# Optimization experiments

Measured on AMD Instinct MI355X. Metric: run time of the kernel, lower is better.

Reference implementation:

```python
import jax, jax.numpy as jnp
import numpy as np

D_MODEL = 1024
HEADS = 16
DILATION = 4
LN_EPS = 1e-5


def setup_inputs() -> dict:
    key = jax.random.key(0)
    ks = jax.random.split(key, 11)
    B, S, D = 2, 4096, D_MODEL
    x = jax.random.normal(ks[0], (B, S, D), dtype=jnp.float32)
    def lin(k):
        kw, kb = jax.random.split(k)
        W = jax.random.normal(kw, (D, D), dtype=jnp.float32) * 0.02  # torch Linear layout [out, in]
        b = jax.random.normal(kb, (D,), dtype=jnp.float32) * 0.02
        return W, b
    Wq, bq = lin(ks[1])
    Wk, bk = lin(ks[2])
    Wv, bv = lin(ks[3])
    Wf, bf = lin(ks[4])
    gamma = jnp.ones((D,), dtype=jnp.float32)
    beta = jnp.zeros((D,), dtype=jnp.float32)
    return {"x": x, "Wq": Wq, "bq": bq, "Wk": Wk, "bk": bk,
            "Wv": Wv, "bv": bv, "Wf": Wf, "bf": bf,
            "gamma": gamma, "beta": beta}


def _layer_norm(x, gamma, beta):
    mu = jnp.mean(x, axis=-1, keepdims=True)
    var = jnp.mean(jnp.square(x - mu), axis=-1, keepdims=True)
    return (x - mu) * jax.lax.rsqrt(var + LN_EPS) * gamma + beta


def reference(x, Wq, bq, Wk, bk, Wv, bv, Wf, bf, gamma, beta):
    B, S, D = x.shape
    dil, H = DILATION, HEADS
    dh = D // H
    pad = (-S) % dil  # padding_size
    xp = jnp.pad(x, ((0, 0), (0, pad), (0, 0)))
    Sp = S + pad
    L = Sp // dil
    # strided (atrous) regrouping: [B, Sp, D] -> [B*dil, L, D]
    xr = xp.reshape(B, L, dil, D).transpose(0, 2, 1, 3).reshape(B * dil, L, D)
    q = xr @ Wq.T + bq
    k = xr @ Wk.T + bk
    v = xr @ Wv.T + bv
    # split heads: [B*dil, H, L, dh]
    q = q.reshape(B * dil, L, H, dh).transpose(0, 2, 1, 3)
    k = k.reshape(B * dil, L, H, dh).transpose(0, 2, 1, 3)
    v = v.reshape(B * dil, L, H, dh).transpose(0, 2, 1, 3)
    scores = jnp.einsum('bhqd,bhkd->bhqk', q, k) / jnp.sqrt(jnp.float32(dh))
    probs = jax.nn.softmax(scores, axis=-1)
    ctx = jnp.einsum('bhqk,bhkd->bhqd', probs, v)
    # merge heads and undo atrous regrouping
    ctx = ctx.transpose(0, 2, 1, 3).reshape(B * dil, L, D)
    ctx = ctx.reshape(B, dil, L, D).transpose(0, 2, 1, 3).reshape(B, Sp, D)
    ctx = ctx[:, :S]
    atted = ctx @ Wf.T + bf  # dropout p=0.0
    final = _layer_norm(atted + x, gamma, beta)
    return (final, atted)
```

## Files before the change

### kernel.cpp

```cpp
#include <hip/hip_runtime.h>
#include <hip/hip_bf16.h>
#include <cstdint>
#include <cstddef>

constexpr int B_  = 2;
constexpr int S_  = 4096;
constexpr int D_  = 1024;
constexpr int H_  = 16;
constexpr int DH_ = 64;
constexpr int DIL = 4;
constexpr int L_  = S_ / DIL;
constexpr int M_  = B_ * S_;

typedef __attribute__((ext_vector_type(8))) short short8;
typedef __attribute__((ext_vector_type(4))) float f32x4;

__device__ __forceinline__ unsigned short f2b(float f) {
    union { float f; unsigned u; } v;
    v.f = f;
    unsigned r = v.u + 0x7fff + ((v.u >> 16) & 1);
    return (unsigned short)(r >> 16);
}

__device__ __forceinline__ unsigned pkbf(float a, float b) {
    float2 t; t.x = a; t.y = b;
    __hip_bfloat162 h = __float22bfloat162_rn(t);
    union { __hip_bfloat162 h; unsigned u; } c; c.h = h;
    return c.u;
}

__device__ __forceinline__ int xcd_swz(int orig, int nwg) {
    int q = nwg >> 3, r = nwg & 7;
    int xcd = orig & 7, idx = orig >> 3;
    return (xcd < r ? xcd * (q + 1) : r * (q + 1) + (xcd - r) * q) + idx;
}

#define GLOAD16(gptr, lptr)                                                    \
    __builtin_amdgcn_global_load_lds(                                          \
        (const __attribute__((address_space(1))) void*)(gptr),                 \
        (__attribute__((address_space(3))) void*)(lptr), 16, 0, 0)

__global__ __launch_bounds__(256)
void conv_f2b(const float* __restrict__ in, unsigned short* __restrict__ out, int n4) {
    int i = blockIdx.x * 256 + threadIdx.x;
    if (i < n4) {
        float4 v = reinterpret_cast<const float4*>(in)[i];
        ushort4 o;
        o.x = f2b(v.x); o.y = f2b(v.y); o.z = f2b(v.z); o.w = f2b(v.w);
        reinterpret_cast<ushort4*>(out)[i] = o;
    }
}

__global__ __launch_bounds__(256)
void conv_w4(const float* __restrict__ w0, const float* __restrict__ w1,
             const float* __restrict__ w2, const float* __restrict__ w3,
             unsigned short* __restrict__ out) {
    int bid = blockIdx.x;
    int which = bid >> 10;
    const float* src = (which == 0) ? w0 : (which == 1) ? w1 : (which == 2) ? w2 : w3;
    int i = (bid & 1023) * 256 + threadIdx.x;
    float4 v = reinterpret_cast<const float4*>(src)[i];
    ushort4 o;
    o.x = f2b(v.x); o.y = f2b(v.y); o.z = f2b(v.z); o.w = f2b(v.w);
    reinterpret_cast<ushort4*>(out + (size_t)which * D_ * D_)[i] = o;
}

template <int OUT_BF16>
__global__ __launch_bounds__(256)
void gemm_mfma(const unsigned short* __restrict__ A,
               const unsigned short* __restrict__ W,
               const float* __restrict__ bias,
               void* __restrict__ Cout, int M, int N, int K) {
    __shared__ unsigned short As[128 * 64];
    __shared__ unsigned short Bs[128 * 64];

    const int tid  = threadIdx.x;
    const int lane = tid & 63, wave = tid >> 6;
    const int l15 = lane & 15, l4 = lane >> 4;
    const int wr = wave >> 1, wc = wave & 1;
    const int gx = N >> 7;
    const int wg = xcd_swz(blockIdx.x, gridDim.x);
    const int bm = (wg / gx) * 128, bn = (wg % gx) * 128;

    f32x4 acc[4][4] = {};

    for (int k0 = 0; k0 < K; k0 += 64) {
        #pragma unroll
        for (int i = 0; i < 4; ++i) {
            int ch = i * 256 + wave * 64 + lane;
            int r = ch >> 3, c8 = ch & 7;
            const unsigned short* ga = A + (size_t)(bm + r) * K + k0 + c8 * 8;
            GLOAD16(ga, (char*)As + (size_t)(i * 256 + wave * 64) * 16);
            const unsigned short* gb = W + (size_t)(bn + r) * K + k0 + c8 * 8;
            GLOAD16(gb, (char*)Bs + (size_t)(i * 256 + wave * 64) * 16);
        }
        __syncthreads();

        #pragma unroll
        for (int ks = 0; ks < 2; ++ks) {
            short8 af[4], bf[4];
            #pragma unroll
            for (int mi = 0; mi < 4; ++mi)
                af[mi] = *reinterpret_cast<const short8*>(
                    &As[(wr * 64 + mi * 16 + l15) * 64 + ks * 32 + l4 * 8]);
            #pragma unroll
            for (int ni = 0; ni < 4; ++ni)
                bf[ni] = *reinterpret_cast<const short8*>(
                    &Bs[(wc * 64 + ni * 16 + l15) * 64 + ks * 32 + l4 * 8]);
            #pragma unroll
            for (int mi = 0; mi < 4; ++mi)
                #pragma unroll
                for (int ni = 0; ni < 4; ++ni)
                    acc[mi][ni] = __builtin_amdgcn_mfma_f32_16x16x32_bf16(
                        af[mi], bf[ni], acc[mi][ni], 0, 0, 0);
        }
        __syncthreads();
    }

    #pragma unroll
    for (int ni = 0; ni < 4; ++ni) {
        int col = bn + wc * 64 + ni * 16 + l15;
        float bv = bias[col];
        #pragma unroll
        for (int mi = 0; mi < 4; ++mi) {
            #pragma unroll
            for (int r = 0; r < 4; ++r) {
                int row = bm + wr * 64 + mi * 16 + l4 * 4 + r;
                float v = acc[mi][ni][r] + bv;
                if (OUT_BF16)
                    ((unsigned short*)Cout)[(size_t)row * N + col] = f2b(v);
                else
                    ((float*)Cout)[(size_t)row * N + col] = v;
            }
        }
    }
}

__global__ __launch_bounds__(256)
void gemm_qkv(const unsigned short* __restrict__ A,
              const unsigned short* __restrict__ W,
              const float* __restrict__ bq, const float* __restrict__ bk,
              const float* __restrict__ bv,
              unsigned short* __restrict__ Qb, unsigned short* __restrict__ Kb,
              unsigned short* __restrict__ Vb, int M, int K) {
    __shared__ unsigned short As[128 * 64];
    __shared__ unsigned short Bs[128 * 64];

    const int tid  = threadIdx.x;
    const int lane = tid & 63, wave = tid >> 6;
    const int l15 = lane & 15, l4 = lane >> 4;
    const int wr = wave >> 1, wc = wave & 1;
    const int gx = 24;
    const int wg = xcd_swz(blockIdx.x, gridDim.x);
    const int bm = (wg / gx) * 128, bn = (wg % gx) * 128;

    f32x4 acc[4][4] = {};

    for (int k0 = 0; k0 < K; k0 += 64) {
        #pragma unroll
        for (int i = 0; i < 4; ++i) {
            int ch = i * 256 + wave * 64 + lane;
            int r = ch >> 3, c8 = ch & 7;
            const unsigned short* ga = A + (size_t)(bm + r) * K + k0 + c8 * 8;
            GLOAD16(ga, (char*)As + (size_t)(i * 256 + wave * 64) * 16);
            const unsigned short* gb = W + (size_t)(bn + r) * K + k0 + c8 * 8;
            GLOAD16(gb, (char*)Bs + (size_t)(i * 256 + wave * 64) * 16);
        }
        __syncthreads();

        #pragma unroll
        for (int ks = 0; ks < 2; ++ks) {
            short8 af[4], bf[4];
            #pragma unroll
            for (int mi = 0; mi < 4; ++mi)
                af[mi] = *reinterpret_cast<const short8*>(
                    &As[(wr * 64 + mi * 16 + l15) * 64 + ks * 32 + l4 * 8]);
            #pragma unroll
            for (int ni = 0; ni < 4; ++ni)
                bf[ni] = *reinterpret_cast<const short8*>(
                    &Bs[(wc * 64 + ni * 16 + l15) * 64 + ks * 32 + l4 * 8]);
            #pragma unroll
            for (int mi = 0; mi < 4; ++mi)
                #pragma unroll
                for (int ni = 0; ni < 4; ++ni)
                    acc[mi][ni] = __builtin_amdgcn_mfma_f32_16x16x32_bf16(
                        af[mi], bf[ni], acc[mi][ni], 0, 0, 0);
        }
        __syncthreads();
    }

    const int seg = bn >> 10;
    const float* bp = (seg == 0) ? bq : (seg == 1) ? bk : bv;
    unsigned short* ob = (seg == 0) ? Qb : (seg == 1) ? Kb : Vb;
    const float qs = (seg == 0) ? 0.125f : 1.0f;
    const int cb = bn & 1023;

    #pragma unroll
    for (int ni = 0; ni < 4; ++ni) {
        int col = cb + wc * 64 + ni * 16 + l15;
        float bvv = bp[col];
        #pragma unroll
        for (int mi = 0; mi < 4; ++mi) {
            #pragma unroll
            for (int r = 0; r < 4; ++r) {
                int row = bm + wr * 64 + mi * 16 + l4 * 4 + r;
                ob[(size_t)row * 1024 + col] = f2b((acc[mi][ni][r] + bvv) * qs);
            }
        }
    }
}

__global__ __launch_bounds__(256)
void tvt(const unsigned short* __restrict__ Vb, unsigned short* __restrict__ Vtg) {
    __shared__ unsigned short Ts[64 * 64];
    const int tid = threadIdx.x;
    const int blk = blockIdx.x;
    const int lt = blk & 15;
    const int h  = (blk >> 4) & 15;
    const int bd = blk >> 8;
    const int b = bd >> 2, dd = bd & 3;
    const size_t rowbase = (size_t)b * S_;

    #pragma unroll
    for (int i = 0; i < 2; ++i) {
        int ch = i * 256 + tid;
        int lloc = ch >> 3, c8 = ch & 7;
        short8 v = *reinterpret_cast<const short8*>(
            Vb + (rowbase + (size_t)(lt * 64 + lloc) * DIL + dd) * D_ + h * 64 + c8 * 8);
        #pragma unroll
        for (int j = 0; j < 8; ++j) {
            int dh = c8 * 8 + j;
            Ts[dh * 64 + (((lloc >> 3) ^ (dh & 7)) * 8) + (lloc & 7)] = (unsigned short)v[j];
        }
    }
    __syncthreads();

    const size_t obase = ((size_t)(bd * 16 + h) * 64) * L_;
    #pragma unroll
    for (int i = 0; i < 2; ++i) {
        int ch = i * 256 + tid;
        int dh = ch >> 3, c = ch & 7;
        uint4 val = *reinterpret_cast<const uint4*>(&Ts[dh * 64 + ((c ^ (dh & 7)) * 8)]);
        *reinterpret_cast<uint4*>(Vtg + obase + (size_t)dh * L_ + lt * 64 + c * 8) = val;
    }
}

__global__ __launch_bounds__(256)
void attn_mfma(const unsigned short* __restrict__ Q,
               const unsigned short* __restrict__ K,
               const unsigned short* __restrict__ Vtg,
               unsigned short* __restrict__ O) {
    __shared__ unsigned short Ks[2][64 * 64];
    __shared__ unsigned short Vs[2][64 * 64];
    __shared__ unsigned short Ps[4][1024];

    const int tid = threadIdx.x;
    const int lane = tid & 63, wave = tid >> 6;
    const int l15 = lane & 15, l4 = lane >> 4;
    const int blk = xcd_swz(blockIdx.x, gridDim.x);
    const int qt = blk & 15;
    const int h  = (blk >> 4) & 15;
    const int bd = blk >> 8;
    const int b = bd >> 2, dd = bd & 3;
    const size_t rowbase = (size_t)b * S_;
    const int colbase = h * DH_;

    short8 qf[2];
    {
        int q = qt * 64 + wave * 16 + l15;
        const unsigned short* qp =
            Q + (rowbase + (size_t)q * DIL + dd) * D_ + colbase;
        qf[0] = *reinterpret_cast<const short8*>(qp + l4 * 8);
        qf[1] = *reinterpret_cast<const short8*>(qp + 32 + l4 * 8);
    }

    const unsigned short* vbase = Vtg + ((size_t)(bd * 16 + h) * 64) * L_;

    auto stageK = [&](int kt, int buf) {
        #pragma unroll
        for (int i = 0; i < 2; ++i) {
            int key = i * 32 + wave * 8 + (lane >> 3);
            int srcc = (lane & 7) ^ (lane >> 3);
            const unsigned short* g =
                K + (rowbase + (size_t)(kt * 64 + key) * DIL + dd) * D_ + colbase + srcc * 8;
            GLOAD16(g, (char*)&Ks[buf][0] + (size_t)(i * 256 + wave * 64) * 16);
        }
    };
    auto stageV = [&](int kt, int buf) {
        #pragma unroll
        for (int i = 0; i < 2; ++i) {
            int dh = i * 32 + wave * 8 + (lane >> 3);
            int srcc = (lane & 7) ^ (lane >> 3);
            const unsigned short* g = vbase + (size_t)dh * L_ + kt * 64 + srcc * 8;
            GLOAD16(g, (char*)&Vs[buf][0] + (size_t)(i * 256 + wave * 64) * 16);
        }
    };

    f32x4 oT[4] = {};
    float m_run = -1e30f, l_run = 0.f;

    stageK(0, 0);
    stageV(0, 0);
    __syncthreads();

    constexpr int NT = L_ / 64;
    for (int kt = 0; kt < NT; ++kt) {
        int cur = kt & 1, nxt = cur ^ 1;
        if (kt < NT - 1) {
            stageK(kt + 1, nxt);
            stageV(kt + 1, nxt);
        }

        f32x4 sT[4];
        #pragma unroll
        for (int n = 0; n < 4; ++n) {
            int row = n * 16 + l15;
            short8 kf0 = *reinterpret_cast<const short8*>(
                &Ks[cur][row * 64 + ((0 * 4 + l4) ^ (l15 & 7)) * 8]);
            short8 kf1 = *reinterpret_cast<const short8*>(
                &Ks[cur][row * 64 + ((1 * 4 + l4) ^ (l15 & 7)) * 8]);
            f32x4 z = {0.f, 0.f, 0.f, 0.f};
            z = __builtin_amdgcn_mfma_f32_16x16x32_bf16(kf0, qf[0], z, 0, 0, 0);
            z = __builtin_amdgcn_mfma_f32_16x16x32_bf16(kf1, qf[1], z, 0, 0, 0);
            sT[n] = z;
        }

        float mx = -1e30f;
        #pragma unroll
        for (int n = 0; n < 4; ++n)
            #pragma unroll
            for (int r = 0; r < 4; ++r) mx = fmaxf(mx, sT[n][r]);
        mx = fmaxf(mx, __shfl_xor(mx, 16));
        mx = fmaxf(mx, __shfl_xor(mx, 32));
        float m_new = fmaxf(m_run, mx);
        float scale = __expf(m_run - m_new);
        float p[4][4], rsum = 0.f;
        #pragma unroll
        for (int n = 0; n < 4; ++n)
            #pragma unroll
            for (int r = 0; r < 4; ++r) {
                p[n][r] = __expf(sT[n][r] - m_new);
                rsum += p[n][r];
            }
        rsum += __shfl_xor(rsum, 16);
        rsum += __shfl_xor(rsum, 32);
        l_run = l_run * scale + rsum;
        m_run = m_new;
        #pragma unroll
        for (int nd = 0; nd < 4; ++nd) oT[nd] *= scale;

        #pragma unroll
        for (int n = 0; n < 4; ++n) {
            uint2 w;
            w.x = pkbf(p[n][0], p[n][1]);
            w.y = pkbf(p[n][2], p[n][3]);
            int c = n * 2 + (l4 >> 1);
            int pc = c ^ (l15 & 7);
            *reinterpret_cast<uint2*>(&Ps[wave][l15 * 64 + pc * 8 + (l4 & 1) * 4]) = w;
        }
        short8 pb0 = *reinterpret_cast<const short8*>(
            &Ps[wave][l15 * 64 + ((0 * 4 + l4) ^ (l15 & 7)) * 8]);
        short8 pb1 = *reinterpret_cast<const short8*>(
            &Ps[wave][l15 * 64 + ((1 * 4 + l4) ^ (l15 & 7)) * 8]);

        #pragma unroll
        for (int ks = 0; ks < 2; ++ks) {
            short8 pb = ks ? pb1 : pb0;
            #pragma unroll
            for (int nd = 0; nd < 4; ++nd) {
                short8 vf = *reinterpret_cast<const short8*>(
                    &Vs[cur][(nd * 16 + l15) * 64 + ((ks * 4 + l4) ^ (l15 & 7)) * 8]);
                oT[nd] = __builtin_amdgcn_mfma_f32_16x16x32_bf16(vf, pb, oT[nd], 0, 0, 0);
            }
        }

        __syncthreads();
    }

    unsigned short* Es = &Ps[0][0];
    float inv = 1.f / l_run;
    #pragma unroll
    for (int nd = 0; nd < 4; ++nd) {
        uint2 w;
        w.x = pkbf(oT[nd][0] * inv, oT[nd][1] * inv);
        w.y = pkbf(oT[nd][2] * inv, oT[nd][3] * inv);
        int chunk = nd * 2 + (l4 >> 1);
        int pc = chunk ^ (l15 & 7);
        *reinterpret_cast<uint2*>(&Es[wave * 1024 + l15 * 64 + pc * 8 + (l4 & 1) * 4]) = w;
    }
    __syncthreads();
    {
        int row = lane >> 2;
        int q = qt * 64 + wave * 16 + row;
        unsigned short* op = O + (rowbase + (size_t)q * DIL + dd) * D_ + colbase;
        #pragma unroll
        for (int i = 0; i < 2; ++i) {
            int c = (lane & 3) * 2 + i;
            int pc = c ^ (row & 7);
            uint4 val = *reinterpret_cast<const uint4*>(&Es[wave * 1024 + row * 64 + pc * 8]);
            *reinterpret_cast<uint4*>(op + c * 8) = val;
        }
    }
}

__global__ __launch_bounds__(256)
void add_ln(const float* __restrict__ atted, const float* __restrict__ x,
            const float* __restrict__ gamma, const float* __restrict__ beta,
            float* __restrict__ out) {
    __shared__ float red[8];
    const int tid = threadIdx.x;
    const size_t base = (size_t)blockIdx.x * D_;

    float4 a  = *reinterpret_cast<const float4*>(atted + base + tid * 4);
    float4 xv = *reinterpret_cast<const float4*>(x + base + tid * 4);
    float v0 = a.x + xv.x, v1 = a.y + xv.y, v2 = a.z + xv.z, v3 = a.w + xv.w;

    float s = v0 + v1 + v2 + v3;
    #pragma unroll
    for (int o = 1; o < 64; o <<= 1) s += __shfl_xor(s, o);
    if ((tid & 63) == 0) red[tid >> 6] = s;
    __syncthreads();
    float mean = (red[0] + red[1] + red[2] + red[3]) * (1.0f / D_);

    float d0 = v0 - mean, d1 = v1 - mean, d2 = v2 - mean, d3 = v3 - mean;
    float sq = d0 * d0 + d1 * d1 + d2 * d2 + d3 * d3;
    #pragma unroll
    for (int o = 1; o < 64; o <<= 1) sq += __shfl_xor(sq, o);
    if ((tid & 63) == 0) red[4 + (tid >> 6)] = sq;
    __syncthreads();
    float var = (red[4] + red[5] + red[6] + red[7]) * (1.0f / D_);
    float inv = rsqrtf(var + 1e-5f);

    float4 g  = *reinterpret_cast<const float4*>(gamma + tid * 4);
    float4 bb = *reinterpret_cast<const float4*>(beta + tid * 4);
    float4 o4;
    o4.x = d0 * inv * g.x + bb.x;
    o4.y = d1 * inv * g.y + bb.y;
    o4.z = d2 * inv * g.z + bb.z;
    o4.w = d3 * inv * g.w + bb.w;
    *reinterpret_cast<float4*>(out + base + tid * 4) = o4;
}

extern "C" void kernel_launch(void* const* d_in, const int* in_sizes, int n_in,
                              void* d_out, int out_size, void* d_ws, size_t ws_size,
                              hipStream_t stream) {
    const float* x     = (const float*)d_in[0];
    const float* Wq    = (const float*)d_in[1];
    const float* bq    = (const float*)d_in[2];
    const float* Wk    = (const float*)d_in[3];
    const float* bk    = (const float*)d_in[4];
    const float* Wv    = (const float*)d_in[5];
    const float* bv    = (const float*)d_in[6];
    const float* Wf    = (const float*)d_in[7];
    const float* bf    = (const float*)d_in[8];
    const float* gamma = (const float*)d_in[9];
    const float* beta  = (const float*)d_in[10];

    float* final_out = (float*)d_out;
    float* atted     = final_out + (size_t)M_ * D_;

    unsigned short* xb  = (unsigned short*)d_ws;
    unsigned short* Wqb = xb  + (size_t)M_ * D_;
    unsigned short* Wkb = Wqb + (size_t)D_ * D_;
    unsigned short* Wvb = Wkb + (size_t)D_ * D_;
    unsigned short* Wfb = Wvb + (size_t)D_ * D_;
    unsigned short* Qb  = Wfb + (size_t)D_ * D_;
    unsigned short* Kb  = Qb  + (size_t)M_ * D_;
    unsigned short* Vb  = Kb  + (size_t)M_ * D_;
    unsigned short* Vtg = Vb  + (size_t)M_ * D_;
    unsigned short* ctxb = xb;

    conv_f2b<<<dim3(M_ * D_ / 4 / 256), 256, 0, stream>>>(x, xb, M_ * D_ / 4);
    conv_w4<<<dim3(4096), 256, 0, stream>>>(Wq, Wk, Wv, Wf, Wqb);

    gemm_qkv<<<dim3((3072 / 128) * (M_ / 128)), 256, 0, stream>>>(
        xb, Wqb, bq, bk, bv, Qb, Kb, Vb, M_, D_);

    tvt<<<dim3(DIL * B_ * H_ * (L_ / 64)), 256, 0, stream>>>(Vb, Vtg);

    attn_mfma<<<dim3(DIL * B_ * H_ * (L_ / 64)), 256, 0, stream>>>(Qb, Kb, Vtg, ctxb);

    gemm_mfma<0><<<dim3((D_ / 128) * (M_ / 128)), 256, 0, stream>>>(
        ctxb, Wfb, bf, atted, M_, D_, D_);

    add_ln<<<dim3(M_), 256, 0, stream>>>(atted, x, gamma, beta, final_out);
}
```

Measured before the change: 317.1 us.

## Double-buffer LDS tiles in GEMM kernels to overlap global loads with MFMA

Both the generic and QKV GEMM kernels now keep two LDS buffers per operand. The next K-tile is issued with direct-to-LDS loads while MFMAs run on the current tile, which removes one barrier per iteration and is meant to hide global-load latency behind compute. LDS use per block doubles to 64KB, which can lower occupancy. Correctness relies on the single end-of-loop barrier also covering completion of the async LDS loads (vmcnt), which the GLOAD16 macro may or may not guarantee.

```diff
diff --git a/kernel.cpp b/kernel.cpp
--- a/kernel.cpp
+++ b/kernel.cpp
@@ -71,8 +71,8 @@
                const unsigned short* __restrict__ W,
                const float* __restrict__ bias,
                void* __restrict__ Cout, int M, int N, int K) {
-    __shared__ unsigned short As[128 * 64];
-    __shared__ unsigned short Bs[128 * 64];
+    __shared__ unsigned short As[2][128 * 64];
+    __shared__ unsigned short Bs[2][128 * 64];
 
     const int tid  = threadIdx.x;
     const int lane = tid & 63, wave = tid >> 6;
@@ -82,19 +82,26 @@
     const int wg = xcd_swz(blockIdx.x, gridDim.x);
     const int bm = (wg / gx) * 128, bn = (wg % gx) * 128;
 
-    f32x4 acc[4][4] = {};
-
-    for (int k0 = 0; k0 < K; k0 += 64) {
+    auto stage = [&](int k0, int buf) {
         #pragma unroll
         for (int i = 0; i < 4; ++i) {
             int ch = i * 256 + wave * 64 + lane;
             int r = ch >> 3, c8 = ch & 7;
             const unsigned short* ga = A + (size_t)(bm + r) * K + k0 + c8 * 8;
-            GLOAD16(ga, (char*)As + (size_t)(i * 256 + wave * 64) * 16);
+            GLOAD16(ga, (char*)&As[buf][0] + (size_t)(i * 256 + wave * 64) * 16);
             const unsigned short* gb = W + (size_t)(bn + r) * K + k0 + c8 * 8;
-            GLOAD16(gb, (char*)Bs + (size_t)(i * 256 + wave * 64) * 16);
-        }
-        __syncthreads();
+            GLOAD16(gb, (char*)&Bs[buf][0] + (size_t)(i * 256 + wave * 64) * 16);
+        }
+    };
+
+    f32x4 acc[4][4] = {};
+
+    stage(0, 0);
+    __syncthreads();
+    int cur = 0;
+
+    for (int k0 = 0; k0 < K; k0 += 64) {
+        if (k0 + 64 < K) stage(k0 + 64, cur ^ 1);
 
         #pragma unroll
         for (int ks = 0; ks < 2; ++ks) {
@@ -102,11 +109,11 @@
             #pragma unroll
             for (int mi = 0; mi < 4; ++mi)
                 af[mi] = *reinterpret_cast<const short8*>(
-                    &As[(wr * 64 + mi * 16 + l15) * 64 + ks * 32 + l4 * 8]);
+                    &As[cur][(wr * 64 + mi * 16 + l15) * 64 + ks * 32 + l4 * 8]);
             #pragma unroll
             for (int ni = 0; ni < 4; ++ni)
                 bf[ni] = *reinterpret_cast<const short8*>(
-                    &Bs[(wc * 64 + ni * 16 + l15) * 64 + ks * 32 + l4 * 8]);
+                    &Bs[cur][(wc * 64 + ni * 16 + l15) * 64 + ks * 32 + l4 * 8]);
             #pragma unroll
             for (int mi = 0; mi < 4; ++mi)
                 #pragma unroll
@@ -115,6 +122,7 @@
                         af[mi], bf[ni], acc[mi][ni], 0, 0, 0);
         }
         __syncthreads();
+        cur ^= 1;
     }
 
     #pragma unroll
@@ -143,8 +151,8 @@
               const float* __restrict__ bv,
               unsigned short* __restrict__ Qb, unsigned short* __restrict__ Kb,
               unsigned short* __restrict__ Vb, int M, int K) {
-    __shared__ unsigned short As[128 * 64];
-    __shared__ unsigned short Bs[128 * 64];
+    __shared__ unsigned short As[2][128 * 64];
+    __shared__ unsigned short Bs[2][128 * 64];
 
     const int tid  = threadIdx.x;
     const int lane = tid & 63, wave = tid >> 6;
@@ -154,19 +162,26 @@
     const int wg = xcd_swz(blockIdx.x, gridDim.x);
     const int bm = (wg / gx) * 128, bn = (wg % gx) * 128;
 
-    f32x4 acc[4][4] = {};
-
-    for (int k0 = 0; k0 < K; k0 += 64) {
+    auto stage = [&](int k0, int buf) {
         #pragma unroll
         for (int i = 0; i < 4; ++i) {
             int ch = i * 256 + wave * 64 + lane;
             int r = ch >> 3, c8 = ch & 7;
             const unsigned short* ga = A + (size_t)(bm + r) * K + k0 + c8 * 8;
-            GLOAD16(ga, (char*)As + (size_t)(i * 256 + wave * 64) * 16);
+            GLOAD16(ga, (char*)&As[buf][0] + (size_t)(i * 256 + wave * 64) * 16);
             const unsigned short* gb = W + (size_t)(bn + r) * K + k0 + c8 * 8;
-            GLOAD16(gb, (char*)Bs + (size_t)(i * 256 + wave * 64) * 16);
-        }
-        __syncthreads();
+            GLOAD16(gb, (char*)&Bs[buf][0] + (size_t)(i * 256 + wave * 64) * 16);
+        }
+    };
+
+    f32x4 acc[4][4] = {};
+
+    stage(0, 0);
+    __syncthreads();
+    int cur = 0;
+
+    for (int k0 = 0; k0 < K; k0 += 64) {
+        if (k0 + 64 < K) stage(k0 + 64, cur ^ 1);
 
         #pragma unroll
         for (int ks = 0; ks < 2; ++ks) {
@@ -174,11 +189,11 @@
             #pragma unroll
             for (int mi = 0; mi < 4; ++mi)
                 af[mi] = *reinterpret_cast<const short8*>(
-                    &As[(wr * 64 + mi * 16 + l15) * 64 + ks * 32 + l4 * 8]);
+                    &As[cur][(wr * 64 + mi * 16 + l15) * 64 + ks * 32 + l4 * 8]);
             #pragma unroll
             for (int ni = 0; ni < 4; ++ni)
                 bf[ni] = *reinterpret_cast<const short8*>(
-                    &Bs[(wc * 64 + ni * 16 + l15) * 64 + ks * 32 + l4 * 8]);
+                    &Bs[cur][(wc * 64 + ni * 16 + l15) * 64 + ks * 32 + l4 * 8]);
             #pragma unroll
             for (int mi = 0; mi < 4; ++mi)
                 #pragma unroll
@@ -187,6 +202,7 @@
                         af[mi], bf[ni], acc[mi][ni], 0, 0, 0);
         }
         __syncthreads();
+        cur ^= 1;
     }
 
     const int seg = bn >> 10;
```

Result: no change. 319.7 us (+0.8%).
